# Kernel optimization log

Hardware: AMD Instinct MI355X
Metric: run time of the kernel (lower is better)

Reference implementation:

```python
import jax, jax.numpy as jnp
import numpy as np

N = 50000      # nodes
E = 800000     # edges (avg degree 16)
D = 512        # in_features
H = 512        # gcn hidden dim (both layers)
G = 64         # graphs in batch
C = 10         # num_classes


def setup_inputs() -> dict:
    key = jax.random.key(0)
    ks = jax.random.split(key, 12)
    x = jax.random.normal(ks[0], (N, D), dtype=jnp.float32)
    edge_index = jax.random.randint(ks[1], (2, E), 0, N, dtype=jnp.int64)
    batch = jnp.sort(jax.random.randint(ks[2], (N,), 0, G, dtype=jnp.int64))
    w = lambda k, sh: (jax.random.normal(k, sh, dtype=jnp.float32) * 0.02)
    return {
        "x": x,
        "edge_index": edge_index,
        "batch": batch,
        # GraphConv layer 0: lin_rel (weight+bias) applied to aggregated neighbors,
        # lin_root (weight, no bias) applied to self features.
        "Wr0": w(ks[3], (D, H)), "br0": jnp.zeros((H,), jnp.float32), "Ws0": w(ks[4], (D, H)),
        # GraphConv layer 1
        "Wr1": w(ks[5], (H, H)), "br1": jnp.zeros((H,), jnp.float32), "Ws1": w(ks[6], (H, H)),
        # final Linear
        "Wl": w(ks[7], (H, C)), "bl": jnp.zeros((C,), jnp.float32),
    }


def _graph_conv(x, src, dst, Wr, br, Ws):
    # sum-aggregate neighbor features: agg[i] = sum_{(j->i) in E} x[j]
    agg = jax.ops.segment_sum(x[src], dst, num_segments=N)  # [N, d_in]
    return agg @ Wr + br + x @ Ws                           # [N, d_out]


def reference(x, edge_index, batch, Wr0, br0, Ws0, Wr1, br1, Ws1, Wl, bl):
    src, dst = edge_index[0], edge_index[1]
    h = jax.nn.relu(_graph_conv(x, src, dst, Wr0, br0, Ws0))   # dropout = identity (eval)
    h = jax.nn.relu(_graph_conv(h, src, dst, Wr1, br1, Ws1))
    # global mean pool over graphs
    sums = jax.ops.segment_sum(h, batch, num_segments=G)                       # [G, H]
    counts = jax.ops.segment_sum(jnp.ones((N, 1), h.dtype), batch, num_segments=G)
    pooled = jax.nn.relu(sums / jnp.maximum(counts, 1.0))
    return pooled @ Wl + bl  # [G, C]
```

## Files before the change

### kernel.cpp

```cpp
#include <hip/hip_runtime.h>

#define NN 50000
#define NE 800000
#define MP 50048
#define GG 64
#define HD 512
#define K2 1024
#define SCAN_BLKS 196

typedef __attribute__((ext_vector_type(8))) short bf16x8;
typedef __attribute__((ext_vector_type(4))) float f32x4;

__device__ __forceinline__ unsigned short f2bf(float f) {
  unsigned u = __builtin_bit_cast(unsigned, f);
  u += 0x7fffu + ((u >> 16) & 1u);
  return (unsigned short)(u >> 16);
}
__device__ __forceinline__ float bf2f(unsigned short h) {
  unsigned u = ((unsigned)h) << 16;
  return __builtin_bit_cast(float, u);
}

__device__ __forceinline__ void g2l16(const void* g, void* l) {
  __builtin_amdgcn_global_load_lds(
      (const __attribute__((address_space(1))) unsigned int*)g,
      (__attribute__((address_space(3))) unsigned int*)l, 16, 0, 0);
}

__global__ __launch_bounds__(256) void prep_kernel(
    const float* __restrict__ x, unsigned short* __restrict__ xb,
    const float* __restrict__ Wr0, const float* __restrict__ Ws0, unsigned short* __restrict__ Wt0,
    const float* __restrict__ Wr1, const float* __restrict__ Ws1, unsigned short* __restrict__ Wt1,
    const int* __restrict__ ei, int* __restrict__ deg) {
  int b = blockIdx.x, t = threadIdx.x;
  if (b < 256) {
    __shared__ float sh[64][65];
    int layer = b >> 7, tl = b & 127;
    int tn = tl >> 4, tk = tl & 15;
    int half = tk >> 3;
    int kw = (tk & 7) * 64, n0 = tn * 64;
    const float* W = layer ? (half ? Ws1 : Wr1) : (half ? Ws0 : Wr0);
    unsigned short* Wt = layer ? Wt1 : Wt0;
    int nn = t & 63;
    int kb = t >> 6;
#pragma unroll
    for (int i = 0; i < 16; i++) {
      int kk = kb + i * 4;
      sh[kk][nn] = W[(size_t)(kw + kk) * HD + n0 + nn];
    }
    __syncthreads();
    int kk2 = t & 63;
#pragma unroll
    for (int i = 0; i < 16; i++) {
      int nn2 = kb + i * 4;
      Wt[(size_t)(n0 + nn2) * K2 + half * HD + kw + kk2] = f2bf(sh[kk2][nn2]);
    }
  } else if (b < 2304) {
    const long long total4 = (long long)MP * HD / 4;
    for (long long i = (long long)(b - 256) * 256 + t; i < total4; i += 2048LL * 256) {
      int r = (int)((i * 4) >> 9);
      float4 v = make_float4(0.f, 0.f, 0.f, 0.f);
      if (r < NN) v = ((const float4*)x)[i];
      ushort4 o;
      o.x = f2bf(v.x); o.y = f2bf(v.y); o.z = f2bf(v.z); o.w = f2bf(v.w);
      ((ushort4*)xb)[i] = o;
    }
  } else {
    for (int i = (b - 2304) * 256 + t; i < NE; i += 512 * 256) {
      atomicAdd(&deg[ei[NE + i]], 1);
    }
  }
}

__global__ __launch_bounds__(256) void scan1_kernel(const int* __restrict__ deg,
                                                    int* __restrict__ tmp,
                                                    int* __restrict__ bsum) {
  __shared__ int sh[256];
  int t = threadIdx.x;
  int i = blockIdx.x * 256 + t;
  int v = (i < NN) ? deg[i] : 0;
  sh[t] = v;
  __syncthreads();
#pragma unroll
  for (int off = 1; off < 256; off <<= 1) {
    int u = (t >= off) ? sh[t - off] : 0;
    __syncthreads();
    sh[t] += u;
    __syncthreads();
  }
  if (i < NN) tmp[i] = sh[t] - v;
  if (t == 255) bsum[blockIdx.x] = sh[255];
}

__global__ __launch_bounds__(256) void scan2_kernel(int* __restrict__ bsum,
                                                    int* __restrict__ row_ptr) {
  __shared__ int sh[256];
  int t = threadIdx.x;
  int v = (t < SCAN_BLKS) ? bsum[t] : 0;
  sh[t] = v;
  __syncthreads();
#pragma unroll
  for (int off = 1; off < 256; off <<= 1) {
    int u = (t >= off) ? sh[t - off] : 0;
    __syncthreads();
    sh[t] += u;
    __syncthreads();
  }
  if (t < SCAN_BLKS) bsum[t] = sh[t] - v;
  if (t == 255) row_ptr[NN] = sh[255];
}

__global__ __launch_bounds__(256) void scan3_kernel(const int* __restrict__ tmp,
                                                    const int* __restrict__ bsum,
                                                    int* __restrict__ row_ptr,
                                                    int* __restrict__ cursor) {
  int i = blockIdx.x * 256 + threadIdx.x;
  if (i < NN) {
    int r = tmp[i] + bsum[blockIdx.x];
    row_ptr[i] = r;
    cursor[i] = r;
  }
}

__global__ void fill_kernel(const int* __restrict__ ei, int* __restrict__ cursor,
                            int* __restrict__ col) {
  int i = blockIdx.x * 256 + threadIdx.x;
  if (i < NE) {
    int d = ei[NE + i];
    int p = atomicAdd(&cursor[d], 1);
    col[p] = ei[i];
  }
}

#define ACC8(v, a)                                        \
  a[0] += bf2f((unsigned short)((v).x & 0xffff));         \
  a[1] += bf2f((unsigned short)((v).x >> 16));            \
  a[2] += bf2f((unsigned short)((v).y & 0xffff));         \
  a[3] += bf2f((unsigned short)((v).y >> 16));            \
  a[4] += bf2f((unsigned short)((v).z & 0xffff));         \
  a[5] += bf2f((unsigned short)((v).z >> 16));            \
  a[6] += bf2f((unsigned short)((v).w & 0xffff));         \
  a[7] += bf2f((unsigned short)((v).w >> 16));

__global__ __launch_bounds__(256) void gather_kernel(const unsigned short* __restrict__ X,
                                                     const int* __restrict__ row_ptr,
                                                     const int* __restrict__ col,
                                                     unsigned short* __restrict__ out) {
  int w = (blockIdx.x * 256 + threadIdx.x) >> 6;
  int lane = threadIdx.x & 63;
  if (w >= MP) return;
  float a[8] = {0.f, 0.f, 0.f, 0.f, 0.f, 0.f, 0.f, 0.f};
  if (w < NN) {
    int r0 = row_ptr[w], r1 = row_ptr[w + 1];
    const unsigned short* Xl = X + lane * 8;
    for (int base = r0; base < r1; base += 64) {
      int idx = base + lane;
      int myc = (idx < r1) ? col[idx] : 0;
      int cnt = min(64, r1 - base);
      int j = 0;
      for (; j + 8 <= cnt; j += 8) {
        int c0 = __shfl(myc, j + 0), c1 = __shfl(myc, j + 1);
        int c2 = __shfl(myc, j + 2), c3 = __shfl(myc, j + 3);
        int c4 = __shfl(myc, j + 4), c5 = __shfl(myc, j + 5);
        int c6 = __shfl(myc, j + 6), c7 = __shfl(myc, j + 7);
        uint4 v0 = *(const uint4*)(Xl + (size_t)c0 * HD);
        uint4 v1 = *(const uint4*)(Xl + (size_t)c1 * HD);
        uint4 v2 = *(const uint4*)(Xl + (size_t)c2 * HD);
        uint4 v3 = *(const uint4*)(Xl + (size_t)c3 * HD);
        uint4 v4 = *(const uint4*)(Xl + (size_t)c4 * HD);
        uint4 v5 = *(const uint4*)(Xl + (size_t)c5 * HD);
        uint4 v6 = *(const uint4*)(Xl + (size_t)c6 * HD);
        uint4 v7 = *(const uint4*)(Xl + (size_t)c7 * HD);
        ACC8(v0, a) ACC8(v1, a) ACC8(v2, a) ACC8(v3, a)
        ACC8(v4, a) ACC8(v5, a) ACC8(v6, a) ACC8(v7, a)
      }
      for (; j < cnt; j++) {
        int c = __shfl(myc, j);
        uint4 v = *(const uint4*)(Xl + (size_t)c * HD);
        ACC8(v, a)
      }
    }
  }
  uint4 o;
  o.x = ((unsigned)f2bf(a[1]) << 16) | f2bf(a[0]);
  o.y = ((unsigned)f2bf(a[3]) << 16) | f2bf(a[2]);
  o.z = ((unsigned)f2bf(a[5]) << 16) | f2bf(a[4]);
  o.w = ((unsigned)f2bf(a[7]) << 16) | f2bf(a[6]);
  *(uint4*)(out + (size_t)w * HD + lane * 8) = o;
}

__global__ __launch_bounds__(512, 2) void gemm_kernel(
    const unsigned short* __restrict__ A0, const unsigned short* __restrict__ A1,
    const unsigned short* __restrict__ Wt, const float* __restrict__ bias,
    unsigned short* __restrict__ Hout) {
  __shared__ __align__(16) unsigned short Ads[128 * 64];
  __shared__ __align__(16) unsigned short Bds[256 * 64];

  const int tid = threadIdx.x;
  const int lane = tid & 63;
  const int wv = tid >> 6;
  const int wm = wv >> 2;
  const int wn = wv & 3;

  const int nwg = 782;
  const int orig = blockIdx.x;
  const int q = nwg >> 3, r8 = nwg & 7;
  const int xcd = orig & 7;
  const int wgid = (xcd < r8 ? xcd * (q + 1) : r8 * (q + 1) + (xcd - r8) * q) + (orig >> 3);

  const int mt = wgid >> 1;
  const int nt = wgid & 1;
  const int row0 = mt * 128;
  const int col0 = nt * 256;

  f32x4 acc[4][4];
#pragma unroll
  for (int i = 0; i < 4; i++)
#pragma unroll
    for (int j = 0; j < 4; j++) acc[i][j] = (f32x4)(0.f);

  const int lr = lane >> 3;
  const int lc = lane & 7;
  const int csw = lc ^ lr;

  for (int kt = 0; kt < 16; ++kt) {
    const int k0 = kt * 64;
    const unsigned short* Asrc = (k0 < HD) ? A0 : A1;
    const int ka = k0 & (HD - 1);
#pragma unroll
    for (int it = 0; it < 2; ++it) {
      int rg = it * 8 + wv;
      g2l16(Asrc + (size_t)(row0 + rg * 8 + lr) * HD + ka + csw * 8, &Ads[rg * 8 * 64]);
    }
#pragma unroll
    for (int it = 0; it < 4; ++it) {
      int rg = it * 8 + wv;
      g2l16(Wt + (size_t)(col0 + rg * 8 + lr) * K2 + k0 + csw * 8, &Bds[rg * 8 * 64]);
    }
    __syncthreads();
#pragma unroll
    for (int kk = 0; kk < 2; ++kk) {
      bf16x8 af[4], bfr[4];
#pragma unroll
      for (int m = 0; m < 4; m++) {
        int r = wm * 64 + m * 16 + (lane & 15);
        int ck = (kk * 4 + (lane >> 4)) ^ (r & 7);
        af[m] = *(const bf16x8*)&Ads[r * 64 + ck * 8];
      }
#pragma unroll
      for (int n = 0; n < 4; n++) {
        int r = wn * 64 + n * 16 + (lane & 15);
        int ck = (kk * 4 + (lane >> 4)) ^ (r & 7);
        bfr[n] = *(const bf16x8*)&Bds[r * 64 + ck * 8];
      }
#pragma unroll
      for (int m = 0; m < 4; m++)
#pragma unroll
        for (int n = 0; n < 4; n++)
          acc[m][n] = __builtin_amdgcn_mfma_f32_16x16x32_bf16(af[m], bfr[n], acc[m][n], 0, 0, 0);
    }
    __syncthreads();
  }

#pragma unroll
  for (int n = 0; n < 4; n++) {
    int c = col0 + wn * 64 + n * 16 + (lane & 15);
    float bv = bias[c];
#pragma unroll
    for (int m = 0; m < 4; m++) {
      int rbase = row0 + wm * 64 + m * 16 + (lane >> 4) * 4;
#pragma unroll
      for (int r = 0; r < 4; r++) {
        float v = acc[m][n][r] + bv;
        v = v > 0.f ? v : 0.f;
        Hout[(size_t)(rbase + r) * HD + c] = f2bf(v);
      }
    }
  }
}

__device__ __forceinline__ int lbound(const int* b, int v) {
  int lo = 0, hi = NN;
  while (lo < hi) { int m = (lo + hi) >> 1; if (b[m] < v) lo = m + 1; else hi = m; }
  return lo;
}

__global__ void pool_kernel(const unsigned short* __restrict__ H, const int* __restrict__ batch,
                            float* __restrict__ pooled) {
  int b = blockIdx.x;
  int g = b >> 4;
  int half = (b >> 3) & 1;
  int chunk = b & 7;
  int col = half * 256 + threadIdx.x;
  int start = lbound(batch, g);
  int end = lbound(batch, g + 1);
  int len = end - start;
  int r0 = start + (int)(((long long)len * chunk) >> 3);
  int r1 = start + (int)(((long long)len * (chunk + 1)) >> 3);
  float s = 0.f;
  for (int r = r0; r < r1; r++) s += bf2f(H[(size_t)r * HD + col]);
  atomicAdd(&pooled[g * HD + col], s);
}

__global__ void final_kernel(const float* __restrict__ pooled, const int* __restrict__ batch,
                             const float* __restrict__ Wl, const float* __restrict__ bl,
                             float* __restrict__ out) {
  int g = blockIdx.x;
  int t = threadIdx.x;
  int lane = t & 63, wv = t >> 6;
  int start = lbound(batch, g);
  int end = lbound(batch, g + 1);
  float cnt = (float)(end - start);
  if (cnt < 1.f) cnt = 1.f;
  float a[10];
#pragma unroll
  for (int c = 0; c < 10; c++) a[c] = 0.f;
  for (int n = t; n < HD; n += 256) {
    float p = pooled[g * HD + n] / cnt;
    p = p > 0.f ? p : 0.f;
#pragma unroll
    for (int c = 0; c < 10; c++) a[c] += p * Wl[n * 10 + c];
  }
  __shared__ float red[10][4];
#pragma unroll
  for (int c = 0; c < 10; c++) {
    float v = a[c];
#pragma unroll
    for (int off = 32; off >= 1; off >>= 1) v += __shfl_down(v, off);
    if (lane == 0) red[c][wv] = v;
  }
  __syncthreads();
  if (t < 10) out[g * 10 + t] = red[t][0] + red[t][1] + red[t][2] + red[t][3] + bl[t];
}

extern "C" void kernel_launch(void* const* d_in, const int* in_sizes, int n_in,
                              void* d_out, int out_size, void* d_ws, size_t ws_size,
                              hipStream_t stream) {
  const float* x   = (const float*)d_in[0];
  const int* ei    = (const int*)d_in[1];
  const int* batch = (const int*)d_in[2];
  const float* Wr0 = (const float*)d_in[3];
  const float* br0 = (const float*)d_in[4];
  const float* Ws0 = (const float*)d_in[5];
  const float* Wr1 = (const float*)d_in[6];
  const float* br1 = (const float*)d_in[7];
  const float* Ws1 = (const float*)d_in[8];
  const float* Wl  = (const float*)d_in[9];
  const float* bl  = (const float*)d_in[10];
  float* out = (float*)d_out;

  char* ws = (char*)d_ws;
  size_t off = 0;
  auto alloc = [&](size_t bytes) { char* p = ws + off; off += (bytes + 255) & ~255ULL; return p; };
  unsigned short* xb   = (unsigned short*)alloc((size_t)MP * HD * 2);
  unsigned short* h0   = (unsigned short*)alloc((size_t)MP * HD * 2);
  unsigned short* aggb = (unsigned short*)alloc((size_t)MP * HD * 2);
  unsigned short* Wt0  = (unsigned short*)alloc((size_t)HD * K2 * 2);
  unsigned short* Wt1  = (unsigned short*)alloc((size_t)HD * K2 * 2);
  float* pooled        = (float*)alloc((size_t)GG * HD * 4);
  int* deg             = (int*)alloc((size_t)NN * 4);
  int* row_ptr         = (int*)alloc((size_t)(NN + 1) * 4);
  int* cursor          = (int*)alloc((size_t)NN * 4);
  int* col             = (int*)alloc((size_t)NE * 4);
  int* stmp            = (int*)alloc((size_t)NN * 4);
  int* bsum            = (int*)alloc((size_t)256 * 4);
  unsigned short* h1 = xb;

  hipMemsetAsync(deg, 0, (size_t)NN * 4, stream);
  hipMemsetAsync(pooled, 0, (size_t)GG * HD * 4, stream);

  prep_kernel<<<2816, 256, 0, stream>>>(x, xb, Wr0, Ws0, Wt0, Wr1, Ws1, Wt1, ei, deg);

  scan1_kernel<<<SCAN_BLKS, 256, 0, stream>>>(deg, stmp, bsum);
  scan2_kernel<<<1, 256, 0, stream>>>(bsum, row_ptr);
  scan3_kernel<<<SCAN_BLKS, 256, 0, stream>>>(stmp, bsum, row_ptr, cursor);
  fill_kernel<<<(NE + 255) / 256, 256, 0, stream>>>(ei, cursor, col);

  gather_kernel<<<MP / 4, 256, 0, stream>>>(xb, row_ptr, col, aggb);
  gemm_kernel<<<782, 512, 0, stream>>>(aggb, xb, Wt0, br0, h0);

  gather_kernel<<<MP / 4, 256, 0, stream>>>(h0, row_ptr, col, aggb);
  gemm_kernel<<<782, 512, 0, stream>>>(aggb, h0, Wt1, br1, h1);

  pool_kernel<<<GG * 16, 256, 0, stream>>>(h1, batch, pooled);
  final_kernel<<<GG, 256, 0, stream>>>(pooled, batch, Wl, bl, out);
}
```

Measured before the change: 662.4 us.

## Double-buffer GEMM LDS tiles with 256x256 blocks and interleaved MFMA scheduling

The GEMM tile grows from 128x256 to 256x256, and the padded row count rises so the grid divides evenly into 392 workgroups with a simpler XCD remap. Global-to-LDS loads are double-buffered: the next-but-one k-tile is issued while MFMAs run on the current buffer, synchronised with vmcnt waits and barriers. MFMA groups are split into quadrants with s_setprio to overlap LDS reads and compute. The larger tile reuses more operands per load but uses 128 KB of LDS and many more accumulator registers, which may drop occupancy to one block per CU.

```diff
diff --git a/kernel.cpp b/kernel.cpp
--- a/kernel.cpp
+++ b/kernel.cpp
@@ -2,7 +2,7 @@
 
 #define NN 50000
 #define NE 800000
-#define MP 50048
+#define MP 50176
 #define GG 64
 #define HD 512
 #define K2 1024
@@ -193,8 +193,8 @@
     const unsigned short* __restrict__ A0, const unsigned short* __restrict__ A1,
     const unsigned short* __restrict__ Wt, const float* __restrict__ bias,
     unsigned short* __restrict__ Hout) {
-  __shared__ __align__(16) unsigned short Ads[128 * 64];
-  __shared__ __align__(16) unsigned short Bds[256 * 64];
+  __shared__ __align__(16) unsigned short Ads[2][256 * 64];
+  __shared__ __align__(16) unsigned short Bds[2][256 * 64];
 
   const int tid = threadIdx.x;
   const int lane = tid & 63;
@@ -202,64 +202,112 @@
   const int wm = wv >> 2;
   const int wn = wv & 3;
 
-  const int nwg = 782;
   const int orig = blockIdx.x;
-  const int q = nwg >> 3, r8 = nwg & 7;
-  const int xcd = orig & 7;
-  const int wgid = (xcd < r8 ? xcd * (q + 1) : r8 * (q + 1) + (xcd - r8) * q) + (orig >> 3);
-
+  const int wgid = (orig & 7) * 49 + (orig >> 3);
   const int mt = wgid >> 1;
   const int nt = wgid & 1;
-  const int row0 = mt * 128;
+  const int row0 = mt * 256;
   const int col0 = nt * 256;
 
-  f32x4 acc[4][4];
-#pragma unroll
-  for (int i = 0; i < 4; i++)
+  f32x4 acc[8][4];
+#pragma unroll
+  for (int i = 0; i < 8; i++)
 #pragma unroll
     for (int j = 0; j < 4; j++) acc[i][j] = (f32x4)(0.f);
 
-  const int lr = lane >> 3;
-  const int lc = lane & 7;
-  const int csw = lc ^ lr;
+  int aoff[4], boff[4];
+#pragma unroll
+  for (int g = 0; g < 4; g++) {
+    int s = g * 512 + tid;
+    int srow = s >> 3, sch = s & 7;
+    int csw = sch ^ (srow & 7);
+    aoff[g] = (row0 + srow) * HD + csw * 8;
+    boff[g] = (col0 + srow) * K2 + csw * 8;
+  }
+
+  auto STAGE = [&](int kt, int buf) {
+    const unsigned short* Asrc = (kt < 8) ? A0 : A1;
+    const int ka = (kt * 64) & (HD - 1);
+    const int k0 = kt * 64;
+#pragma unroll
+    for (int g = 0; g < 4; g++)
+      g2l16(Asrc + aoff[g] + ka, &Ads[buf][(g * 512 + wv * 64) * 8]);
+#pragma unroll
+    for (int g = 0; g < 4; g++)
+      g2l16(Wt + boff[g] + k0, &Bds[buf][(g * 512 + wv * 64) * 8]);
+  };
+
+  auto rdA = [&](int buf, int m, int kk) -> bf16x8 {
+    int r = wm * 128 + m * 16 + (lane & 15);
+    int ck = (kk * 4 + (lane >> 4)) ^ (r & 7);
+    return *(const bf16x8*)&Ads[buf][r * 64 + ck * 8];
+  };
+  auto rdB = [&](int buf, int n, int kk) -> bf16x8 {
+    int r = wn * 64 + n * 16 + (lane & 15);
+    int ck = (kk * 4 + (lane >> 4)) ^ (r & 7);
+    return *(const bf16x8*)&Bds[buf][r * 64 + ck * 8];
+  };
+
+  STAGE(0, 0);
+  STAGE(1, 1);
+  asm volatile("s_waitcnt vmcnt(8)" ::: "memory");
+  __builtin_amdgcn_s_barrier();
 
   for (int kt = 0; kt < 16; ++kt) {
-    const int k0 = kt * 64;
-    const unsigned short* Asrc = (k0 < HD) ? A0 : A1;
-    const int ka = k0 & (HD - 1);
-#pragma unroll
-    for (int it = 0; it < 2; ++it) {
-      int rg = it * 8 + wv;
-      g2l16(Asrc + (size_t)(row0 + rg * 8 + lr) * HD + ka + csw * 8, &Ads[rg * 8 * 64]);
-    }
-#pragma unroll
-    for (int it = 0; it < 4; ++it) {
-      int rg = it * 8 + wv;
-      g2l16(Wt + (size_t)(col0 + rg * 8 + lr) * K2 + k0 + csw * 8, &Bds[rg * 8 * 64]);
-    }
-    __syncthreads();
-#pragma unroll
-    for (int kk = 0; kk < 2; ++kk) {
-      bf16x8 af[4], bfr[4];
-#pragma unroll
-      for (int m = 0; m < 4; m++) {
-        int r = wm * 64 + m * 16 + (lane & 15);
-        int ck = (kk * 4 + (lane >> 4)) ^ (r & 7);
-        af[m] = *(const bf16x8*)&Ads[r * 64 + ck * 8];
-      }
-#pragma unroll
-      for (int n = 0; n < 4; n++) {
-        int r = wn * 64 + n * 16 + (lane & 15);
-        int ck = (kk * 4 + (lane >> 4)) ^ (r & 7);
-        bfr[n] = *(const bf16x8*)&Bds[r * 64 + ck * 8];
-      }
-#pragma unroll
-      for (int m = 0; m < 4; m++)
-#pragma unroll
-        for (int n = 0; n < 4; n++)
-          acc[m][n] = __builtin_amdgcn_mfma_f32_16x16x32_bf16(af[m], bfr[n], acc[m][n], 0, 0, 0);
-    }
-    __syncthreads();
+    const int cur = kt & 1;
+    bf16x8 fa0[4][2], fa1[4][2], fb0[2][2], fb1[2][2];
+#pragma unroll
+    for (int m = 0; m < 4; m++) { fa0[m][0] = rdA(cur, m, 0); fa0[m][1] = rdA(cur, m, 1); }
+#pragma unroll
+    for (int n = 0; n < 2; n++) { fb0[n][0] = rdB(cur, n, 0); fb0[n][1] = rdB(cur, n, 1); }
+    __builtin_amdgcn_s_setprio(1);
+#pragma unroll
+    for (int m = 0; m < 4; m++)
+#pragma unroll
+      for (int n = 0; n < 2; n++) {
+        acc[m][n] = __builtin_amdgcn_mfma_f32_16x16x32_bf16(fa0[m][0], fb0[n][0], acc[m][n], 0, 0, 0);
+        acc[m][n] = __builtin_amdgcn_mfma_f32_16x16x32_bf16(fa0[m][1], fb0[n][1], acc[m][n], 0, 0, 0);
+      }
+    __builtin_amdgcn_s_setprio(0);
+#pragma unroll
+    for (int n = 0; n < 2; n++) { fb1[n][0] = rdB(cur, n + 2, 0); fb1[n][1] = rdB(cur, n + 2, 1); }
+    __builtin_amdgcn_s_setprio(1);
+#pragma unroll
+    for (int m = 0; m < 4; m++)
+#pragma unroll
+      for (int n = 0; n < 2; n++) {
+        acc[m][n + 2] = __builtin_amdgcn_mfma_f32_16x16x32_bf16(fa0[m][0], fb1[n][0], acc[m][n + 2], 0, 0, 0);
+        acc[m][n + 2] = __builtin_amdgcn_mfma_f32_16x16x32_bf16(fa0[m][1], fb1[n][1], acc[m][n + 2], 0, 0, 0);
+      }
+    __builtin_amdgcn_s_setprio(0);
+#pragma unroll
+    for (int m = 0; m < 4; m++) { fa1[m][0] = rdA(cur, m + 4, 0); fa1[m][1] = rdA(cur, m + 4, 1); }
+    __builtin_amdgcn_s_setprio(1);
+#pragma unroll
+    for (int m = 0; m < 4; m++)
+#pragma unroll
+      for (int n = 0; n < 2; n++) {
+        acc[m + 4][n + 2] = __builtin_amdgcn_mfma_f32_16x16x32_bf16(fa1[m][0], fb1[n][0], acc[m + 4][n + 2], 0, 0, 0);
+        acc[m + 4][n + 2] = __builtin_amdgcn_mfma_f32_16x16x32_bf16(fa1[m][1], fb1[n][1], acc[m + 4][n + 2], 0, 0, 0);
+      }
+    __builtin_amdgcn_s_setprio(0);
+    __builtin_amdgcn_s_barrier();
+    if (kt < 14) STAGE(kt + 2, cur);
+    __builtin_amdgcn_s_setprio(1);
+#pragma unroll
+    for (int m = 0; m < 4; m++)
+#pragma unroll
+      for (int n = 0; n < 2; n++) {
+        acc[m + 4][n] = __builtin_amdgcn_mfma_f32_16x16x32_bf16(fa1[m][0], fb0[n][0], acc[m + 4][n], 0, 0, 0);
+        acc[m + 4][n] = __builtin_amdgcn_mfma_f32_16x16x32_bf16(fa1[m][1], fb0[n][1], acc[m + 4][n], 0, 0, 0);
+      }
+    __builtin_amdgcn_s_setprio(0);
+    if (kt < 14) {
+      asm volatile("s_waitcnt vmcnt(8)" ::: "memory");
+    } else {
+      asm volatile("s_waitcnt vmcnt(0)" ::: "memory");
+    }
+    __builtin_amdgcn_s_barrier();
   }
 
 #pragma unroll
@@ -267,8 +315,8 @@
     int c = col0 + wn * 64 + n * 16 + (lane & 15);
     float bv = bias[c];
 #pragma unroll
-    for (int m = 0; m < 4; m++) {
-      int rbase = row0 + wm * 64 + m * 16 + (lane >> 4) * 4;
+    for (int m = 0; m < 8; m++) {
+      int rbase = row0 + wm * 128 + m * 16 + (lane >> 4) * 4;
 #pragma unroll
       for (int r = 0; r < 4; r++) {
         float v = acc[m][n][r] + bv;
@@ -377,10 +425,10 @@
   fill_kernel<<<(NE + 255) / 256, 256, 0, stream>>>(ei, cursor, col);
 
   gather_kernel<<<MP / 4, 256, 0, stream>>>(xb, row_ptr, col, aggb);
-  gemm_kernel<<<782, 512, 0, stream>>>(aggb, xb, Wt0, br0, h0);
+  gemm_kernel<<<392, 512, 0, stream>>>(aggb, xb, Wt0, br0, h0);
 
   gather_kernel<<<MP / 4, 256, 0, stream>>>(h0, row_ptr, col, aggb);
-  gemm_kernel<<<782, 512, 0, stream>>>(aggb, h0, Wt1, br1, h1);
+  gemm_kernel<<<392, 512, 0, stream>>>(aggb, h0, Wt1, br1, h1);
 
   pool_kernel<<<GG * 16, 256, 0, stream>>>(h1, batch, pooled);
   final_kernel<<<GG, 256, 0, stream>>>(pooled, batch, Wl, bl, out);
```

New measurement: 692.9 us. +4.6%, slower.

## Partition gather by feature column slices per XCD and use 16-bit column indices

Applied to the files above, without the earlier changes.

The neighbor-sum gather is restructured so each block handles a 32-column slice of the feature matrix, two slices per XCD chosen from blockIdx. The intent is that each XCD's L2 only holds its own column slice of X, turning most random row reads into L2 hits instead of HBM or MALL traffic. Within a row, 8 lanes read 64-byte segments for 8 edges at once and the partial sums are combined with xor shuffles. The CSR column array is stored as 16-bit indices, which holds because N is below 65536, halving index traffic. The cost is that the row pointers and indices are re-read once per slice, each edge fetch is small, and the locality gain depends on blocks being dispatched round-robin across XCDs.

```diff
diff --git a/kernel.cpp b/kernel.cpp
--- a/kernel.cpp
+++ b/kernel.cpp
@@ -123,70 +123,60 @@
 }
 
 __global__ void fill_kernel(const int* __restrict__ ei, int* __restrict__ cursor,
-                            int* __restrict__ col) {
+                            unsigned short* __restrict__ colu) {
   int i = blockIdx.x * 256 + threadIdx.x;
   if (i < NE) {
     int d = ei[NE + i];
     int p = atomicAdd(&cursor[d], 1);
-    col[p] = ei[i];
-  }
-}
-
-#define ACC8(v, a)                                        \
-  a[0] += bf2f((unsigned short)((v).x & 0xffff));         \
-  a[1] += bf2f((unsigned short)((v).x >> 16));            \
-  a[2] += bf2f((unsigned short)((v).y & 0xffff));         \
-  a[3] += bf2f((unsigned short)((v).y >> 16));            \
-  a[4] += bf2f((unsigned short)((v).z & 0xffff));         \
-  a[5] += bf2f((unsigned short)((v).z >> 16));            \
-  a[6] += bf2f((unsigned short)((v).w & 0xffff));         \
-  a[7] += bf2f((unsigned short)((v).w >> 16));
+    colu[p] = (unsigned short)ei[i];
+  }
+}
 
 __global__ __launch_bounds__(256) void gather_kernel(const unsigned short* __restrict__ X,
                                                      const int* __restrict__ row_ptr,
-                                                     const int* __restrict__ col,
+                                                     const unsigned short* __restrict__ colu,
                                                      unsigned short* __restrict__ out) {
-  int w = (blockIdx.x * 256 + threadIdx.x) >> 6;
-  int lane = threadIdx.x & 63;
-  if (w >= MP) return;
-  float a[8] = {0.f, 0.f, 0.f, 0.f, 0.f, 0.f, 0.f, 0.f};
-  if (w < NN) {
-    int r0 = row_ptr[w], r1 = row_ptr[w + 1];
-    const unsigned short* Xl = X + lane * 8;
-    for (int base = r0; base < r1; base += 64) {
-      int idx = base + lane;
-      int myc = (idx < r1) ? col[idx] : 0;
-      int cnt = min(64, r1 - base);
-      int j = 0;
-      for (; j + 8 <= cnt; j += 8) {
-        int c0 = __shfl(myc, j + 0), c1 = __shfl(myc, j + 1);
-        int c2 = __shfl(myc, j + 2), c3 = __shfl(myc, j + 3);
-        int c4 = __shfl(myc, j + 4), c5 = __shfl(myc, j + 5);
-        int c6 = __shfl(myc, j + 6), c7 = __shfl(myc, j + 7);
-        uint4 v0 = *(const uint4*)(Xl + (size_t)c0 * HD);
-        uint4 v1 = *(const uint4*)(Xl + (size_t)c1 * HD);
-        uint4 v2 = *(const uint4*)(Xl + (size_t)c2 * HD);
-        uint4 v3 = *(const uint4*)(Xl + (size_t)c3 * HD);
-        uint4 v4 = *(const uint4*)(Xl + (size_t)c4 * HD);
-        uint4 v5 = *(const uint4*)(Xl + (size_t)c5 * HD);
-        uint4 v6 = *(const uint4*)(Xl + (size_t)c6 * HD);
-        uint4 v7 = *(const uint4*)(Xl + (size_t)c7 * HD);
-        ACC8(v0, a) ACC8(v1, a) ACC8(v2, a) ACC8(v3, a)
-        ACC8(v4, a) ACC8(v5, a) ACC8(v6, a) ACC8(v7, a)
-      }
-      for (; j < cnt; j++) {
-        int c = __shfl(myc, j);
-        uint4 v = *(const uint4*)(Xl + (size_t)c * HD);
-        ACC8(v, a)
-      }
-    }
-  }
-  uint4 o;
-  o.x = ((unsigned)f2bf(a[1]) << 16) | f2bf(a[0]);
-  o.y = ((unsigned)f2bf(a[3]) << 16) | f2bf(a[2]);
-  o.z = ((unsigned)f2bf(a[5]) << 16) | f2bf(a[4]);
-  o.w = ((unsigned)f2bf(a[7]) << 16) | f2bf(a[6]);
-  *(uint4*)(out + (size_t)w * HD + lane * 8) = o;
+  const int b = blockIdx.x;
+  const int t = threadIdx.x;
+  const int xcd = b & 7, rb = b >> 3;
+  const int wv = t >> 6, lane = t & 63;
+  const int sub = lane & 7;
+  const int grp = lane >> 3;
+  const int rstart = rb * 391;
+
+  for (int ph = 0; ph < 2; ph++) {
+    const int s = xcd * 2 + ph;
+    const unsigned short* Xs = X + s * 32 + sub * 4;
+    for (int r = rstart + wv; r < rstart + 391; r += 4) {
+      float a0 = 0.f, a1 = 0.f, a2 = 0.f, a3 = 0.f;
+      int r0 = 0, r1 = 0;
+      if (r < NN) { r0 = row_ptr[r]; r1 = row_ptr[r + 1]; }
+      for (int base = r0; base < r1; base += 8) {
+        int e = base + grp;
+        if (e < r1) {
+          int c = colu[e];
+          uint2 v = *(const uint2*)(Xs + (size_t)c * HD);
+          a0 += bf2f((unsigned short)(v.x & 0xffff));
+          a1 += bf2f((unsigned short)(v.x >> 16));
+          a2 += bf2f((unsigned short)(v.y & 0xffff));
+          a3 += bf2f((unsigned short)(v.y >> 16));
+        }
+      }
+#pragma unroll
+      for (int off = 8; off < 64; off <<= 1) {
+        a0 += __shfl_xor(a0, off);
+        a1 += __shfl_xor(a1, off);
+        a2 += __shfl_xor(a2, off);
+        a3 += __shfl_xor(a3, off);
+      }
+      if (grp == 0) {
+        uint2 o;
+        o.x = ((unsigned)f2bf(a1) << 16) | f2bf(a0);
+        o.y = ((unsigned)f2bf(a3) << 16) | f2bf(a2);
+        *(uint2*)(out + (size_t)r * HD + s * 32 + sub * 4) = o;
+      }
+    }
+  }
 }
 
 __global__ __launch_bounds__(512, 2) void gemm_kernel(
@@ -361,7 +351,7 @@
   int* deg             = (int*)alloc((size_t)NN * 4);
   int* row_ptr         = (int*)alloc((size_t)(NN + 1) * 4);
   int* cursor          = (int*)alloc((size_t)NN * 4);
-  int* col             = (int*)alloc((size_t)NE * 4);
+  unsigned short* colu = (unsigned short*)alloc((size_t)NE * 2);
   int* stmp            = (int*)alloc((size_t)NN * 4);
   int* bsum            = (int*)alloc((size_t)256 * 4);
   unsigned short* h1 = xb;
@@ -374,12 +364,12 @@
   scan1_kernel<<<SCAN_BLKS, 256, 0, stream>>>(deg, stmp, bsum);
   scan2_kernel<<<1, 256, 0, stream>>>(bsum, row_ptr);
   scan3_kernel<<<SCAN_BLKS, 256, 0, stream>>>(stmp, bsum, row_ptr, cursor);
-  fill_kernel<<<(NE + 255) / 256, 256, 0, stream>>>(ei, cursor, col);
-
-  gather_kernel<<<MP / 4, 256, 0, stream>>>(xb, row_ptr, col, aggb);
+  fill_kernel<<<(NE + 255) / 256, 256, 0, stream>>>(ei, cursor, colu);
+
+  gather_kernel<<<1024, 256, 0, stream>>>(xb, row_ptr, colu, aggb);
   gemm_kernel<<<782, 512, 0, stream>>>(aggb, xb, Wt0, br0, h0);
 
-  gather_kernel<<<MP / 4, 256, 0, stream>>>(h0, row_ptr, col, aggb);
+  gather_kernel<<<1024, 256, 0, stream>>>(h0, row_ptr, colu, aggb);
   gemm_kernel<<<782, 512, 0, stream>>>(aggb, h0, Wt1, br1, h1);
 
   pool_kernel<<<GG * 16, 256, 0, stream>>>(h1, batch, pooled);
```

Result: slower. 1.264 ms (+90.9%).

## Fuse mean pooling into second GEMM epilogue and use 16-bit column indices

Applied to the files above, without the earlier changes.

The second-layer GEMM now accumulates relu outputs into per-graph sums, first through LDS atomics and then global atomics, instead of writing h1 and running a separate pool kernel. CSR column indices are stored as uint16 to halve index traffic in the gathers, and the pooled-buffer memset is folded into the prep kernel. This removes a full activation write and re-read, at the cost of atomic contention in the epilogue. The uint16 indices depend on the node count staying below 65536.

```diff
diff --git a/kernel.cpp b/kernel.cpp
--- a/kernel.cpp
+++ b/kernel.cpp
@@ -31,7 +31,7 @@
     const float* __restrict__ x, unsigned short* __restrict__ xb,
     const float* __restrict__ Wr0, const float* __restrict__ Ws0, unsigned short* __restrict__ Wt0,
     const float* __restrict__ Wr1, const float* __restrict__ Ws1, unsigned short* __restrict__ Wt1,
-    const int* __restrict__ ei, int* __restrict__ deg) {
+    const int* __restrict__ ei, int* __restrict__ deg, float* __restrict__ pooled) {
   int b = blockIdx.x, t = threadIdx.x;
   if (b < 256) {
     __shared__ float sh[64][65];
@@ -65,10 +65,13 @@
       o.x = f2bf(v.x); o.y = f2bf(v.y); o.z = f2bf(v.z); o.w = f2bf(v.w);
       ((ushort4*)xb)[i] = o;
     }
-  } else {
+  } else if (b < 2816) {
     for (int i = (b - 2304) * 256 + t; i < NE; i += 512 * 256) {
       atomicAdd(&deg[ei[NE + i]], 1);
     }
+  } else {
+    int i = (b - 2816) * 256 + t;
+    if (i < GG * HD / 4) ((float4*)pooled)[i] = make_float4(0.f, 0.f, 0.f, 0.f);
   }
 }
 
@@ -123,12 +126,12 @@
 }
 
 __global__ void fill_kernel(const int* __restrict__ ei, int* __restrict__ cursor,
-                            int* __restrict__ col) {
+                            unsigned short* __restrict__ colu) {
   int i = blockIdx.x * 256 + threadIdx.x;
   if (i < NE) {
     int d = ei[NE + i];
     int p = atomicAdd(&cursor[d], 1);
-    col[p] = ei[i];
+    colu[p] = (unsigned short)ei[i];
   }
 }
 
@@ -144,7 +147,7 @@
 
 __global__ __launch_bounds__(256) void gather_kernel(const unsigned short* __restrict__ X,
                                                      const int* __restrict__ row_ptr,
-                                                     const int* __restrict__ col,
+                                                     const unsigned short* __restrict__ colu,
                                                      unsigned short* __restrict__ out) {
   int w = (blockIdx.x * 256 + threadIdx.x) >> 6;
   int lane = threadIdx.x & 63;
@@ -155,7 +158,7 @@
     const unsigned short* Xl = X + lane * 8;
     for (int base = r0; base < r1; base += 64) {
       int idx = base + lane;
-      int myc = (idx < r1) ? col[idx] : 0;
+      int myc = (idx < r1) ? (int)colu[idx] : 0;
       int cnt = min(64, r1 - base);
       int j = 0;
       for (; j + 8 <= cnt; j += 8) {
@@ -189,10 +192,12 @@
   *(uint4*)(out + (size_t)w * HD + lane * 8) = o;
 }
 
+template <bool DOPOOL>
 __global__ __launch_bounds__(512, 2) void gemm_kernel(
     const unsigned short* __restrict__ A0, const unsigned short* __restrict__ A1,
     const unsigned short* __restrict__ Wt, const float* __restrict__ bias,
-    unsigned short* __restrict__ Hout) {
+    unsigned short* __restrict__ Hout, const int* __restrict__ batch,
+    float* __restrict__ pooled) {
   __shared__ __align__(16) unsigned short Ads[128 * 64];
   __shared__ __align__(16) unsigned short Bds[256 * 64];
 
@@ -262,18 +267,51 @@
     __syncthreads();
   }
 
-#pragma unroll
-  for (int n = 0; n < 4; n++) {
-    int c = col0 + wn * 64 + n * 16 + (lane & 15);
-    float bv = bias[c];
-#pragma unroll
-    for (int m = 0; m < 4; m++) {
-      int rbase = row0 + wm * 64 + m * 16 + (lane >> 4) * 4;
-#pragma unroll
-      for (int r = 0; r < 4; r++) {
-        float v = acc[m][n][r] + bv;
-        v = v > 0.f ? v : 0.f;
-        Hout[(size_t)(rbase + r) * HD + c] = f2bf(v);
+  if constexpr (DOPOOL) {
+    float* pbuf = (float*)Ads;
+    for (int i = tid; i < 8 * 256; i += 512) pbuf[i] = 0.f;
+    const int gfirst = batch[row0];
+    __syncthreads();
+#pragma unroll
+    for (int n = 0; n < 4; n++) {
+      int c = col0 + wn * 64 + n * 16 + (lane & 15);
+      float bv = bias[c];
+#pragma unroll
+      for (int m = 0; m < 4; m++) {
+        int rbase = row0 + wm * 64 + m * 16 + (lane >> 4) * 4;
+#pragma unroll
+        for (int r = 0; r < 4; r++) {
+          int row = rbase + r;
+          if (row < NN) {
+            float v = acc[m][n][r] + bv;
+            v = v > 0.f ? v : 0.f;
+            int slot = batch[row] - gfirst;
+            if (slot < 8) atomicAdd(&pbuf[slot * 256 + (c - col0)], v);
+            else atomicAdd(&pooled[(size_t)batch[row] * HD + c], v);
+          }
+        }
+      }
+    }
+    __syncthreads();
+    for (int i = tid; i < 8 * 256; i += 512) {
+      float v = pbuf[i];
+      int g = gfirst + (i >> 8);
+      if (v != 0.f && g < GG) atomicAdd(&pooled[(size_t)g * HD + col0 + (i & 255)], v);
+    }
+  } else {
+#pragma unroll
+    for (int n = 0; n < 4; n++) {
+      int c = col0 + wn * 64 + n * 16 + (lane & 15);
+      float bv = bias[c];
+#pragma unroll
+      for (int m = 0; m < 4; m++) {
+        int rbase = row0 + wm * 64 + m * 16 + (lane >> 4) * 4;
+#pragma unroll
+        for (int r = 0; r < 4; r++) {
+          float v = acc[m][n][r] + bv;
+          v = v > 0.f ? v : 0.f;
+          Hout[(size_t)(rbase + r) * HD + c] = f2bf(v);
+        }
       }
     }
   }
@@ -283,23 +321,6 @@
   int lo = 0, hi = NN;
   while (lo < hi) { int m = (lo + hi) >> 1; if (b[m] < v) lo = m + 1; else hi = m; }
   return lo;
-}
-
-__global__ void pool_kernel(const unsigned short* __restrict__ H, const int* __restrict__ batch,
-                            float* __restrict__ pooled) {
-  int b = blockIdx.x;
-  int g = b >> 4;
-  int half = (b >> 3) & 1;
-  int chunk = b & 7;
-  int col = half * 256 + threadIdx.x;
-  int start = lbound(batch, g);
-  int end = lbound(batch, g + 1);
-  int len = end - start;
-  int r0 = start + (int)(((long long)len * chunk) >> 3);
-  int r1 = start + (int)(((long long)len * (chunk + 1)) >> 3);
-  float s = 0.f;
-  for (int r = r0; r < r1; r++) s += bf2f(H[(size_t)r * HD + col]);
-  atomicAdd(&pooled[g * HD + col], s);
 }
 
 __global__ void final_kernel(const float* __restrict__ pooled, const int* __restrict__ batch,
@@ -361,27 +382,24 @@
   int* deg             = (int*)alloc((size_t)NN * 4);
   int* row_ptr         = (int*)alloc((size_t)(NN + 1) * 4);
   int* cursor          = (int*)alloc((size_t)NN * 4);
-  int* col             = (int*)alloc((size_t)NE * 4);
+  unsigned short* colu = (unsigned short*)alloc((size_t)NE * 2);
   int* stmp            = (int*)alloc((size_t)NN * 4);
   int* bsum            = (int*)alloc((size_t)256 * 4);
-  unsigned short* h1 = xb;
 
   hipMemsetAsync(deg, 0, (size_t)NN * 4, stream);
-  hipMemsetAsync(pooled, 0, (size_t)GG * HD * 4, stream);
-
-  prep_kernel<<<2816, 256, 0, stream>>>(x, xb, Wr0, Ws0, Wt0, Wr1, Ws1, Wt1, ei, deg);
+
+  prep_kernel<<<2848, 256, 0, stream>>>(x, xb, Wr0, Ws0, Wt0, Wr1, Ws1, Wt1, ei, deg, pooled);
 
   scan1_kernel<<<SCAN_BLKS, 256, 0, stream>>>(deg, stmp, bsum);
   scan2_kernel<<<1, 256, 0, stream>>>(bsum, row_ptr);
   scan3_kernel<<<SCAN_BLKS, 256, 0, stream>>>(stmp, bsum, row_ptr, cursor);
-  fill_kernel<<<(NE + 255) / 256, 256, 0, stream>>>(ei, cursor, col);
-
-  gather_kernel<<<MP / 4, 256, 0, stream>>>(xb, row_ptr, col, aggb);
-  gemm_kernel<<<782, 512, 0, stream>>>(aggb, xb, Wt0, br0, h0);
-
-  gather_kernel<<<MP / 4, 256, 0, stream>>>(h0, row_ptr, col, aggb);
-  gemm_kernel<<<782, 512, 0, stream>>>(aggb, h0, Wt1, br1, h1);
-
-  pool_kernel<<<GG * 16, 256, 0, stream>>>(h1, batch, pooled);
+  fill_kernel<<<(NE + 255) / 256, 256, 0, stream>>>(ei, cursor, colu);
+
+  gather_kernel<<<MP / 4, 256, 0, stream>>>(xb, row_ptr, colu, aggb);
+  gemm_kernel<false><<<782, 512, 0, stream>>>(aggb, xb, Wt0, br0, h0, batch, pooled);
+
+  gather_kernel<<<MP / 4, 256, 0, stream>>>(h0, row_ptr, colu, aggb);
+  gemm_kernel<true><<<782, 512, 0, stream>>>(aggb, h0, Wt1, br1, nullptr, batch, pooled);
+
   final_kernel<<<GG, 256, 0, stream>>>(pooled, batch, Wl, bl, out);
 }
```

Result: slower. 781.8 us (+18.0%).
